# Performance work log

Hardware: AMD Instinct MI355X
Metric: run time of the kernel (lower is better)

Reference implementation:

```python
import jax, jax.numpy as jnp
import numpy as np

N_BATCH = 4096
D_FEAT = 64
N_CLASSES = 10
DET_EPS = 1e-8


def setup_inputs() -> dict:
    key = jax.random.key(0)
    k1, k2, k3 = jax.random.split(key, 3)
    # small-magnitude means and variances bounded away from 0 keep the
    # KL values (and hence sigmoid(KL)) in a numerically meaningful range
    mu = jax.random.normal(k1, (N_BATCH, D_FEAT), dtype=jnp.float32) * 0.1
    var = jax.random.uniform(k2, (N_BATCH, D_FEAT), dtype=jnp.float32) + 0.5
    labels = jax.random.randint(k3, (N_BATCH,), 0, N_CLASSES)
    return {"mu": mu, "var": var, "labels": labels}


def _pairwise_kl(mu, var):
    """K[i, j] = KL(N(mu_i, diag(var_i)) || N(mu_j, diag(var_j))),
    matching the original's kl_mvn on the row/col tiling, but computed
    elementwise/matmul instead of dense diag_embed + inv/det (same math:
    inv(diag(S1)) @ diag(S0) summed == sum(S0/S1); det(diag(S)) == prod(S))."""
    D = mu.shape[1]
    inv_var = 1.0 / var                                   # [N, D]
    # tr term: sum_d var_i,d / var_j,d
    tr = var @ inv_var.T                                  # [N, N]
    # det term: det(S1)/ (det(S0)+eps) with diagonal determinants = products
    p = jnp.prod(var, axis=1)                             # [N]
    det = p[None, :] / (p[:, None] + DET_EPS)             # [N, N]
    # quad term: sum_d (mu_j - mu_i)^2 / var_j,d, expanded into matmuls
    mu_sq = mu * mu                                       # [N, D]
    quad = (mu_sq @ inv_var.T
            - 2.0 * (mu @ (mu * inv_var).T)
            + jnp.sum(mu_sq * inv_var, axis=1)[None, :])  # [N, N]
    return 0.5 * (tr + det + quad - D)


def reference(mu, var, labels):
    N = mu.shape[0]
    K = _pairwise_kl(mu, var)                 # KL(i -> j)
    sym = 0.5 * (K + K.T)                     # symmetric_kl over the pair grid
    logits = jax.nn.sigmoid(sym)              # [N, N]

    same = labels[:, None] == labels[None, :]
    off_diag = ~jnp.eye(N, dtype=bool)        # logits_mask: zero out diagonal
    p_mask = (same & off_diag).astype(logits.dtype)
    n_mask = ((~same) & off_diag).astype(logits.dtype)

    pos = logits * p_mask
    neg = logits * n_mask
    return (jnp.mean(pos), jnp.mean(neg), jnp.sum(pos), jnp.sum(neg))
```

## Files before the change

### kernel.cpp

```cpp
#include <hip/hip_runtime.h>


#define N 4096
#define D 64
#define KH 256
#define MT 128
#define TILES2 32
#define NBLK2 528
#define DET_EPS 1e-8f

typedef short bf16x8 __attribute__((ext_vector_type(8)));
typedef float f32x16 __attribute__((ext_vector_type(16)));

#define WS_H    0
#define WS_PSL  (N * KH * 2)
#define WS_PART (WS_PSL + N * 16)

static __device__ __forceinline__ unsigned short f2bf(float x) {
  unsigned int u = __float_as_uint(x);
  unsigned int r = (u + 0x7FFFu + ((u >> 16) & 1u)) >> 16;
  return (unsigned short)r;
}

static __device__ __forceinline__ f32x16 mfma_bf16(bf16x8 a, bf16x8 b, f32x16 c) {
  return __builtin_amdgcn_mfma_f32_32x32x16_bf16(a, b, c, 0, 0, 0);
}

__global__ __launch_bounds__(256) void precompute_kernel(
    const float* __restrict__ mu, const float* __restrict__ var,
    const int* __restrict__ labels,
    unsigned short* __restrict__ Hf, float4* __restrict__ PSL) {
  const int t = threadIdx.x;
  const int lane = t & 63;
  const int w = t >> 6;
  const int r = blockIdx.x * 4 + w;

  const float m = mu[r * D + lane];
  const float v = var[r * D + lane];
  const float g0 = 1.0f / v;
  const float f0 = v + m * m;
  const float f1 = -2.0f * m;
  const float g1 = m * g0;

  const size_t base = (size_t)(r >> 5) * 8192 + (size_t)(lane >> 2) * 512
                      + (size_t)(r & 31) * 16 + (size_t)(lane & 3) * 4;
  *(ushort4*)&Hf[base] = make_ushort4(f2bf(f0), f2bf(f1), f2bf(g0), f2bf(g1));

  float p = v;
  float s = m * m * g0;
  #pragma unroll
  for (int off = 1; off < 64; off <<= 1) {
    p *= __shfl_xor(p, off);
    s += __shfl_xor(s, off);
  }
  if (lane == 0) {
    PSL[r] = make_float4(p, 1.0f / (p + DET_EPS), 0.25f * s - 16.0f,
                         (float)labels[r]);
  }
}

__global__ __launch_bounds__(256, 2) void pair_kernel(
    const unsigned short* __restrict__ Hf,
    const float4* __restrict__ PSL, float* __restrict__ partial) {
  __shared__ float4 sPi[128];
  __shared__ float4 sPj[128];
  __shared__ float red[8];

  int L = (int)blockIdx.x;
  int it = (int)(32.5f - sqrtf(32.5f * 32.5f - 2.0f * (float)L));
  while (it > 0 && L < it * TILES2 - it * (it - 1) / 2) --it;
  while (L >= (it + 1) * TILES2 - (it + 1) * it / 2) ++it;
  const int jt = it + (L - (it * TILES2 - it * (it - 1) / 2));
  const int i0 = it * MT, j0 = jt * MT;

  const int t = threadIdx.x;
  const int lane = t & 63;
  const int w = t >> 6;
  const int sr = w >> 1, sc = w & 1;

  if (t < 128) sPi[t] = PSL[i0 + t];
  else sPj[t - 128] = PSL[j0 + t - 128];
  __syncthreads();

  const int l31 = lane & 31;
  const int slot = l31 * 16 + (lane >> 5) * 8;
  const unsigned short* pa = Hf + (size_t)(i0 / 32 + sr * 2) * 8192 + slot;
  const unsigned short* pb = Hf + (size_t)(j0 / 32 + sc * 2) * 8192 + slot;

  const bool active = !(it == jt && w == 2);

  f32x16 C00 = {}, C01 = {}, C10 = {}, C11 = {};
  float pos = 0.0f, neg = 0.0f;

  if (active) {
    #pragma unroll 4
    for (int k = 0; k < 16; ++k) {
      const bf16x8 a0 = *(const bf16x8*)(pa + k * 512);
      const bf16x8 a1 = *(const bf16x8*)(pa + 8192 + k * 512);
      const bf16x8 c0 = *(const bf16x8*)(pb + k * 512);
      const bf16x8 c1 = *(const bf16x8*)(pb + 8192 + k * 512);
      const bf16x8 b0 = __builtin_shufflevector(c0, c0, 2, 3, 0, 1, 6, 7, 4, 5);
      const bf16x8 b1 = __builtin_shufflevector(c1, c1, 2, 3, 0, 1, 6, 7, 4, 5);
      C00 = mfma_bf16(a0, b0, C00);
      C01 = mfma_bf16(a0, b1, C01);
      C10 = mfma_bf16(a1, b0, C10);
      C11 = mfma_bf16(a1, b1, C11);
    }

    const int rbase = 4 * (lane >> 5);
    #pragma unroll
    for (int mn = 0; mn < 4; ++mn) {
      const int m = mn >> 1, n = mn & 1;
      const f32x16 C = (mn == 0) ? C00 : (mn == 1) ? C01 : (mn == 2) ? C10 : C11;
      const int jloc = (sc * 2 + n) * 32 + l31;
      const int j = j0 + jloc;
      const float4 pj = sPj[jloc];
      #pragma unroll
      for (int r = 0; r < 16; ++r) {
        const int row = (r & 3) + 8 * (r >> 2) + rbase;
        const int iloc = (sr * 2 + m) * 32 + row;
        const int i = i0 + iloc;
        if (i < j) {
          const float4 pi = sPi[iloc];
          const float det = pj.x * pi.y + pi.x * pj.y;
          const float sym = 0.25f * (C[r] + det) + pi.z + pj.z;
          const float sig = __builtin_amdgcn_rcpf(1.0f + __expf(-sym));
          if (pi.w == pj.w) pos += sig; else neg += sig;
        }
      }
    }
  }

  #pragma unroll
  for (int off = 32; off > 0; off >>= 1) {
    pos += __shfl_down(pos, off);
    neg += __shfl_down(neg, off);
  }
  if (lane == 0) { red[w] = pos; red[4 + w] = neg; }
  __syncthreads();
  if (t == 0) {
    partial[L]         = red[0] + red[1] + red[2] + red[3];
    partial[NBLK2 + L] = red[4] + red[5] + red[6] + red[7];
  }
}

__global__ __launch_bounds__(256) void finalize_kernel(
    const float* __restrict__ partial, float* __restrict__ out) {
  __shared__ float redp[4], redn[4];
  const int t = threadIdx.x;
  const int lane = t & 63, w = t >> 6;
  float p = 0.0f, n = 0.0f;
  for (int i = t; i < NBLK2; i += 256) {
    p += partial[i];
    n += partial[NBLK2 + i];
  }
  #pragma unroll
  for (int off = 32; off > 0; off >>= 1) {
    p += __shfl_down(p, off);
    n += __shfl_down(n, off);
  }
  if (lane == 0) { redp[w] = p; redn[w] = n; }
  __syncthreads();
  if (t == 0) {
    const float pos = 2.0f * (redp[0] + redp[1] + redp[2] + redp[3]);
    const float neg = 2.0f * (redn[0] + redn[1] + redn[2] + redn[3]);
    out[0] = pos * (1.0f / 16777216.0f);
    out[1] = neg * (1.0f / 16777216.0f);
    out[2] = pos;
    out[3] = neg;
  }
}

extern "C" void kernel_launch(void* const* d_in, const int* in_sizes, int n_in,
                              void* d_out, int out_size, void* d_ws, size_t ws_size,
                              hipStream_t stream) {
  const float* mu = (const float*)d_in[0];
  const float* var = (const float*)d_in[1];
  const int* labels = (const int*)d_in[2];
  float* out = (float*)d_out;
  char* ws = (char*)d_ws;

  unsigned short* Hf = (unsigned short*)(ws + WS_H);
  float4* PSL = (float4*)(ws + WS_PSL);
  float* partial = (float*)(ws + WS_PART);

  precompute_kernel<<<dim3(N / 4), dim3(256), 0, stream>>>(mu, var, labels, Hf, PSL);
  pair_kernel<<<dim3(NBLK2), dim3(256), 0, stream>>>(Hf, PSL, partial);
  finalize_kernel<<<dim3(1), dim3(256), 0, stream>>>(partial, out);
}
```

Baseline: 78.68 us.

## Stage operand tiles in LDS via async global_load_lds double buffering

```diff
diff --git a/kernel.cpp b/kernel.cpp
--- a/kernel.cpp
+++ b/kernel.cpp
@@ -24,6 +24,13 @@
 
 static __device__ __forceinline__ f32x16 mfma_bf16(bf16x8 a, bf16x8 b, f32x16 c) {
   return __builtin_amdgcn_mfma_f32_32x32x16_bf16(a, b, c, 0, 0, 0);
+}
+
+static __device__ __forceinline__ void glds16(const unsigned short* g,
+                                              unsigned short* l) {
+  __builtin_amdgcn_global_load_lds(
+      (const __attribute__((address_space(1))) unsigned int*)g,
+      (__attribute__((address_space(3))) unsigned int*)l, 16, 0, 0);
 }
 
 __global__ __launch_bounds__(256) void precompute_kernel(
@@ -62,6 +69,7 @@
 __global__ __launch_bounds__(256, 2) void pair_kernel(
     const unsigned short* __restrict__ Hf,
     const float4* __restrict__ PSL, float* __restrict__ partial) {
+  __shared__ unsigned short sH[2][2][4][4][512];
   __shared__ float4 sPi[128];
   __shared__ float4 sPj[128];
   __shared__ float red[8];
@@ -77,36 +85,59 @@
   const int lane = t & 63;
   const int w = t >> 6;
   const int sr = w >> 1, sc = w & 1;
+  const int at0 = i0 >> 5, bt0 = j0 >> 5;
 
   if (t < 128) sPi[t] = PSL[i0 + t];
   else sPj[t - 128] = PSL[j0 + t - 128];
+
+#define STAGE(buf, q)                                                       \
+  {                                                                         \
+    _Pragma("unroll")                                                       \
+    for (int u = 0; u < 8; ++u) {                                           \
+      const int cid = w * 8 + u;                                            \
+      const int p = cid >> 4, rt = (cid >> 2) & 3, kk = cid & 3;            \
+      const unsigned short* g = Hf                                          \
+          + (size_t)((p ? bt0 : at0) + rt) * 8192 + ((q) * 4 + kk) * 512    \
+          + lane * 8;                                                       \
+      glds16(g, &sH[buf][p][rt][kk][0]);                                    \
+    }                                                                       \
+  }
+
+  STAGE(0, 0);
   __syncthreads();
 
   const int l31 = lane & 31;
   const int slot = l31 * 16 + (lane >> 5) * 8;
-  const unsigned short* pa = Hf + (size_t)(i0 / 32 + sr * 2) * 8192 + slot;
-  const unsigned short* pb = Hf + (size_t)(j0 / 32 + sc * 2) * 8192 + slot;
 
   const bool active = !(it == jt && w == 2);
 
   f32x16 C00 = {}, C01 = {}, C10 = {}, C11 = {};
   float pos = 0.0f, neg = 0.0f;
 
+  #pragma unroll
+  for (int q = 0; q < 4; ++q) {
+    const int cb = q & 1;
+    if (q < 3) STAGE(cb ^ 1, q + 1);
+    if (active) {
+      #pragma unroll
+      for (int kk = 0; kk < 4; ++kk) {
+        const bf16x8 a0 = *(const bf16x8*)&sH[cb][0][2 * sr + 0][kk][slot];
+        const bf16x8 a1 = *(const bf16x8*)&sH[cb][0][2 * sr + 1][kk][slot];
+        const bf16x8 c0 = *(const bf16x8*)&sH[cb][1][2 * sc + 0][kk][slot];
+        const bf16x8 c1 = *(const bf16x8*)&sH[cb][1][2 * sc + 1][kk][slot];
+        const bf16x8 b0 = __builtin_shufflevector(c0, c0, 2, 3, 0, 1, 6, 7, 4, 5);
+        const bf16x8 b1 = __builtin_shufflevector(c1, c1, 2, 3, 0, 1, 6, 7, 4, 5);
+        C00 = mfma_bf16(a0, b0, C00);
+        C01 = mfma_bf16(a0, b1, C01);
+        C10 = mfma_bf16(a1, b0, C10);
+        C11 = mfma_bf16(a1, b1, C11);
+      }
+    }
+    __syncthreads();
+  }
+#undef STAGE
+
   if (active) {
-    #pragma unroll 4
-    for (int k = 0; k < 16; ++k) {
-      const bf16x8 a0 = *(const bf16x8*)(pa + k * 512);
-      const bf16x8 a1 = *(const bf16x8*)(pa + 8192 + k * 512);
-      const bf16x8 c0 = *(const bf16x8*)(pb + k * 512);
-      const bf16x8 c1 = *(const bf16x8*)(pb + 8192 + k * 512);
-      const bf16x8 b0 = __builtin_shufflevector(c0, c0, 2, 3, 0, 1, 6, 7, 4, 5);
-      const bf16x8 b1 = __builtin_shufflevector(c1, c1, 2, 3, 0, 1, 6, 7, 4, 5);
-      C00 = mfma_bf16(a0, b0, C00);
-      C01 = mfma_bf16(a0, b1, C01);
-      C10 = mfma_bf16(a1, b0, C10);
-      C11 = mfma_bf16(a1, b1, C11);
-    }
-
     const int rbase = 4 * (lane >> 5);
     #pragma unroll
     for (int mn = 0; mn < 4; ++mn) {
```

Measured after the change: 86.58 us. +10.0%, slower.
